# Optimization experiments

Measured on AMD Instinct MI355X. Metric: run time of the kernel, lower is better.

Reference implementation:

```python
import jax, jax.numpy as jnp
import numpy as np

B, N, D = 4, 2048, 2048
H, KVH, DH = 16, 4, 128  # query heads, kv heads (GQA), head dim
SCALE = DH ** -0.5
NEG = -jnp.finfo(jnp.float32).max


def setup_inputs() -> dict:
    key = jax.random.key(0)
    ks = jax.random.split(key, 5)
    s = 1.0 / np.sqrt(D)  # fan-in scaling for bias-free Linear weights
    return {
        "x": jax.random.normal(ks[0], (B, N, D), dtype=jnp.float32),
        "Wq": jax.random.normal(ks[1], (D, H * DH), dtype=jnp.float32) * s,
        "Wk": jax.random.normal(ks[2], (D, KVH * DH), dtype=jnp.float32) * s,
        "Wv": jax.random.normal(ks[3], (D, KVH * DH), dtype=jnp.float32) * s,
        "Wo": jax.random.normal(ks[4], (H * DH, D), dtype=jnp.float32) * s,
    }


def reference(x, Wq, Wk, Wv, Wo):
    # projections (bias-free Linear), split into heads: b n (h d) -> b h n d
    q = (x @ Wq).reshape(B, N, H, DH).transpose(0, 2, 1, 3)
    k = (x @ Wk).reshape(B, N, KVH, DH).transpose(0, 2, 1, 3)
    v = (x @ Wv).reshape(B, N, KVH, DH).transpose(0, 2, 1, 3)
    # GQA head repeat: 'b kvh n d -> b (r kvh) n d' with r outermost == tile
    r = H // KVH
    k = jnp.tile(k, (1, r, 1, 1))
    v = jnp.tile(v, (1, r, 1, 1))
    # scaled dot-product attention, causal triu(1) mask, softmax in fp32
    dots = jnp.einsum("bhid,bhjd->bhij", q, k) * SCALE
    causal_mask = jnp.triu(jnp.ones((N, N), dtype=bool), k=1)
    dots = jnp.where(causal_mask, NEG, dots)
    attn = jax.nn.softmax(dots.astype(jnp.float32), axis=-1).astype(dots.dtype)
    out = jnp.einsum("bhij,bhjd->bhid", attn, v)
    # merge heads: b h n d -> b n (h d), then output projection
    out = out.transpose(0, 2, 1, 3).reshape(B, N, H * DH)
    return out @ Wo
```

## Files before the change

kernel.cpp:

```cpp
#include <hip/hip_runtime.h>

#define B_   4
#define N_   2048
#define D_   2048
#define H_   16
#define KVH_ 4
#define DH_  128
#define SCALE_ 0.08838834764831845f
#define NEGF_ (-1.0e30f)

typedef __bf16 bf16x8 __attribute__((ext_vector_type(8)));
typedef float  f32x4  __attribute__((ext_vector_type(4)));
typedef unsigned short ushort_t;

typedef __attribute__((address_space(1))) const void* gas_cp;
typedef __attribute__((address_space(3))) void* las_p;

__device__ __forceinline__ void gload_lds16(const void* g, void* l) {
  __builtin_amdgcn_global_load_lds((gas_cp)g, (las_p)l, 16, 0, 0);
}

__device__ __forceinline__ ushort_t f2bf(float f) {
  union { float f; unsigned u; } c;
  c.f = f;
  unsigned u = c.u;
  u += 0x7fffu + ((u >> 16) & 1u);
  return (ushort_t)(u >> 16);
}

__device__ __forceinline__ float bf2f(ushort_t u) {
  union { unsigned u; float f; } c;
  c.u = ((unsigned)u) << 16;
  return c.f;
}

__global__ __launch_bounds__(256) void cvt_f32_bf16_k(
    const float* __restrict__ in, ushort_t* __restrict__ out, int n) {
  int i = (blockIdx.x * 256 + threadIdx.x) * 4;
  if (i >= n) return;
  float4 v = *reinterpret_cast<const float4*>(in + i);
  ushort4 o;
  o.x = f2bf(v.x); o.y = f2bf(v.y); o.z = f2bf(v.z); o.w = f2bf(v.w);
  *reinterpret_cast<ushort4*>(out + i) = o;
}

__global__ __launch_bounds__(256) void tconv_k(
    const float* __restrict__ src, ushort_t* __restrict__ dst, int K, int N) {
  __shared__ float tile[32][33];
  int n0 = blockIdx.x * 32, k0 = blockIdx.y * 32;
  int tx = threadIdx.x, ty = threadIdx.y;
#pragma unroll
  for (int i = 0; i < 32; i += 8)
    tile[ty + i][tx] = src[(size_t)(k0 + ty + i) * N + n0 + tx];
  __syncthreads();
#pragma unroll
  for (int i = 0; i < 32; i += 8)
    dst[(size_t)(n0 + ty + i) * K + k0 + tx] = f2bf(tile[tx][ty + i]);
}

__global__ __launch_bounds__(256) void vt_k(
    const ushort_t* __restrict__ qkv, ushort_t* __restrict__ vtg) {
  __shared__ ushort_t tile[32][33];
  int n0 = blockIdx.x * 32, d0 = blockIdx.y * 32, g = blockIdx.z;
  int b = g >> 2, kvh = g & 3;
  int tx = threadIdx.x, ty = threadIdx.y;
  const ushort_t* src = qkv + (size_t)(b * N_) * 3072 + 2560 + kvh * 128;
#pragma unroll
  for (int i = 0; i < 32; i += 8)
    tile[ty + i][tx] = src[(size_t)(n0 + ty + i) * 3072 + d0 + tx];
  __syncthreads();
  ushort_t* dst = vtg + (size_t)(g * 128) * 2048;
#pragma unroll
  for (int i = 0; i < 32; i += 8)
    dst[(size_t)(d0 + ty + i) * 2048 + n0 + tx] = tile[tx][ty + i];
}

template <int OUTF32>
__global__ __launch_bounds__(256, 2) void gemm_bt_k(
    const ushort_t* __restrict__ A, const ushort_t* __restrict__ Bt,
    void* __restrict__ C, int M, int N, int K) {
  __shared__ ushort_t As[128 * 64];
  __shared__ ushort_t Bs[128 * 64];
  const int tid = threadIdx.x;
  const int wave = tid >> 6, lane = tid & 63;
  const int lo = lane & 15, hi = lane >> 4;
  const int wm = wave >> 1, wn = wave & 1;
  const int nwg = gridDim.x * gridDim.y;
  const int id = blockIdx.y * gridDim.x + blockIdx.x;
  const int swz = (id & 7) * (nwg >> 3) + (id >> 3);
  const int m0 = (swz / gridDim.x) * 128, n0 = (swz % gridDim.x) * 128;

  f32x4 acc[4][4] = {};

  const int sr = lane >> 3;
  const int sc = lane & 7;

  const int kTiles = K >> 6;
  for (int kt = 0; kt < kTiles; ++kt) {
    const int k0 = kt << 6;
    __syncthreads();
#pragma unroll
    for (int j = 0; j < 4; ++j) {
      int r = wave * 32 + j * 8 + sr;
      int cs = sc ^ (r & 7);
      gload_lds16(A  + (size_t)(m0 + r) * K + k0 + cs * 8, As + (wave * 32 + j * 8) * 64);
      gload_lds16(Bt + (size_t)(n0 + r) * K + k0 + cs * 8, Bs + (wave * 32 + j * 8) * 64);
    }
    __syncthreads();
#pragma unroll
    for (int ks = 0; ks < 2; ++ks) {
      bf16x8 af[4], bfr[4];
#pragma unroll
      for (int mi = 0; mi < 4; ++mi) {
        int r = wm * 64 + mi * 16 + lo;
        int cs = ((ks << 2) | hi) ^ (r & 7);
        af[mi] = *reinterpret_cast<const bf16x8*>(As + r * 64 + cs * 8);
      }
#pragma unroll
      for (int ni = 0; ni < 4; ++ni) {
        int r = wn * 64 + ni * 16 + lo;
        int cs = ((ks << 2) | hi) ^ (r & 7);
        bfr[ni] = *reinterpret_cast<const bf16x8*>(Bs + r * 64 + cs * 8);
      }
#pragma unroll
      for (int mi = 0; mi < 4; ++mi)
#pragma unroll
        for (int ni = 0; ni < 4; ++ni)
          acc[mi][ni] = __builtin_amdgcn_mfma_f32_16x16x32_bf16(af[mi], bfr[ni], acc[mi][ni], 0, 0, 0);
    }
  }
#pragma unroll
  for (int mi = 0; mi < 4; ++mi) {
#pragma unroll
    for (int ni = 0; ni < 4; ++ni) {
#pragma unroll
      for (int r = 0; r < 4; ++r) {
        int row = m0 + wm * 64 + mi * 16 + hi * 4 + r;
        int col = n0 + wn * 64 + ni * 16 + lo;
        float v = acc[mi][ni][r];
        if (OUTF32) reinterpret_cast<float*>(C)[(size_t)row * N + col] = v;
        else        reinterpret_cast<ushort_t*>(C)[(size_t)row * N + col] = f2bf(v);
      }
    }
  }
}

__global__ __launch_bounds__(256, 2) void attn_k(
    const ushort_t* __restrict__ qkv, const ushort_t* __restrict__ vtg,
    ushort_t* __restrict__ ob) {
  __shared__ ushort_t Ks[2][64 * 128];
  __shared__ ushort_t Vs[2][128 * 64];
  __shared__ ushort_t Pl[4][32 * 40];

  const int nqb = gridDim.x - 1 - blockIdx.x;
  const int bh = blockIdx.y;
  const int b = bh >> 4, h = bh & 15, kvh = h & 3;
  const int tid = threadIdx.x, wave = tid >> 6, lane = tid & 63;
  const int lo = lane & 15, hi = lane >> 4;
  const int q0w = nqb * 128 + wave * 32;

  const ushort_t* qbase = qkv + (size_t)(b * N_) * 3072;
  const ushort_t* kbase = qbase + 2048 + kvh * 128;
  const ushort_t* vbase = vtg + (size_t)((b * 4 + kvh) * 128) * 2048;

  bf16x8 qf[2][4];
#pragma unroll
  for (int mi = 0; mi < 2; ++mi) {
    const ushort_t* qrow = qbase + (size_t)(q0w + mi * 16 + lo) * 3072 + h * 128;
#pragma unroll
    for (int kf = 0; kf < 4; ++kf) {
      union { bf16x8 v; ushort_t s[8]; } t;
      t.v = *reinterpret_cast<const bf16x8*>(qrow + kf * 32 + hi * 8);
#pragma unroll
      for (int j = 0; j < 8; ++j) t.s[j] = f2bf(bf2f(t.s[j]) * SCALE_);
      qf[mi][kf] = t.v;
    }
  }

  float m[2] = {NEGF_, NEGF_};
  float l[2] = {0.f, 0.f};
  f32x4 o[2][8] = {};

  const int nk = (nqb + 1) * 2;

  auto STAGE = [&](int k0, int bufi) {
#pragma unroll
    for (int j = 0; j < 4; ++j) {
      int ci = j * 256 + tid;
      int r = ci >> 4, c = ci & 15;
      gload_lds16(kbase + (size_t)(k0 + r) * 3072 + (c ^ (r & 7)) * 8,
                  &Ks[bufi][(j * 256 + wave * 64) * 8]);
    }
#pragma unroll
    for (int j = 0; j < 4; ++j) {
      int ci = j * 256 + tid;
      int r = ci >> 3, c = ci & 7;
      gload_lds16(vbase + (size_t)r * 2048 + k0 + (c ^ (r & 7)) * 8,
                  &Vs[bufi][(j * 256 + wave * 64) * 8]);
    }
  };

  STAGE(0, 0);
  __syncthreads();
  int cur = 0;

  for (int kt = 0; kt < nk; ++kt) {
    const int k0 = kt * 64;
    if (kt + 1 < nk) STAGE(k0 + 64, cur ^ 1);

    const bool act = (k0 < q0w + 32);
    if (act) {
      f32x4 s[2][4] = {};
#pragma unroll
      for (int cf = 0; cf < 4; ++cf) {
        int r = cf * 16 + lo;
        bf16x8 kb[4];
#pragma unroll
        for (int kf = 0; kf < 4; ++kf) {
          int cc = ((kf << 2) | hi) ^ (r & 7);
          kb[kf] = *reinterpret_cast<const bf16x8*>(&Ks[cur][r * 128 + cc * 8]);
        }
#pragma unroll
        for (int mi = 0; mi < 2; ++mi)
#pragma unroll
          for (int kf = 0; kf < 4; ++kf)
            s[mi][cf] = __builtin_amdgcn_mfma_f32_16x16x32_bf16(kb[kf], qf[mi][kf], s[mi][cf], 0, 0, 0);
      }
#pragma unroll
      for (int mi = 0; mi < 2; ++mi) {
        const int qrow = q0w + mi * 16 + lo;
        const bool domask = (k0 + 63 > q0w + mi * 16);
        float mx = NEGF_;
#pragma unroll
        for (int cf = 0; cf < 4; ++cf)
#pragma unroll
          for (int r = 0; r < 4; ++r) {
            float v = s[mi][cf][r];
            if (domask && (k0 + cf * 16 + hi * 4 + r > qrow)) v = NEGF_;
            s[mi][cf][r] = v;
            mx = fmaxf(mx, v);
          }
        mx = fmaxf(mx, __shfl_xor(mx, 16, 64));
        mx = fmaxf(mx, __shfl_xor(mx, 32, 64));
        float mn = fmaxf(m[mi], mx);
        float sc = __expf(m[mi] - mn);
        m[mi] = mn;
        float ps = 0.f;
#pragma unroll
        for (int cf = 0; cf < 4; ++cf)
#pragma unroll
          for (int r = 0; r < 4; ++r) {
            float p = __expf(s[mi][cf][r] - mn);
            ps += p;
            s[mi][cf][r] = p;
          }
        ps += __shfl_xor(ps, 16, 64);
        ps += __shfl_xor(ps, 32, 64);
        l[mi] = l[mi] * sc + ps;
        int bsrc = (lane & 48) | (hi << 2);
#pragma unroll
        for (int r = 0; r < 4; ++r) {
          float sb = __shfl(sc, bsrc + r, 64);
#pragma unroll
          for (int f = 0; f < 8; ++f) o[mi][f][r] *= sb;
        }
      }
#pragma unroll
      for (int ks = 0; ks < 2; ++ks) {
#pragma unroll
        for (int mi = 0; mi < 2; ++mi)
#pragma unroll
          for (int c2 = 0; c2 < 2; ++c2) {
            int cf = ks * 2 + c2;
            unsigned w0 = (unsigned)f2bf(s[mi][cf][0]) | ((unsigned)f2bf(s[mi][cf][1]) << 16);
            unsigned w1 = (unsigned)f2bf(s[mi][cf][2]) | ((unsigned)f2bf(s[mi][cf][3]) << 16);
            uint2 w; w.x = w0; w.y = w1;
            *reinterpret_cast<uint2*>(&Pl[wave][(mi * 16 + lo) * 40 + c2 * 16 + hi * 4]) = w;
          }
        bf16x8 pa[2];
#pragma unroll
        for (int mi = 0; mi < 2; ++mi)
          pa[mi] = *reinterpret_cast<const bf16x8*>(&Pl[wave][(mi * 16 + lo) * 40 + hi * 8]);
#pragma unroll
        for (int f = 0; f < 8; ++f) {
          int d = f * 16 + lo;
          int cc = ((ks << 2) | hi) ^ (d & 7);
          bf16x8 vb = *reinterpret_cast<const bf16x8*>(&Vs[cur][d * 64 + cc * 8]);
#pragma unroll
          for (int mi = 0; mi < 2; ++mi)
            o[mi][f] = __builtin_amdgcn_mfma_f32_16x16x32_bf16(pa[mi], vb, o[mi][f], 0, 0, 0);
        }
      }
    }
    __syncthreads();
    cur ^= 1;
  }

  ushort_t* obase = ob + (size_t)(b * N_ + q0w) * 2048 + h * 128;
#pragma unroll
  for (int mi = 0; mi < 2; ++mi) {
    float invl = 1.0f / l[mi];
    int bsrc = (lane & 48) | (hi << 2);
    float ib[4];
#pragma unroll
    for (int r = 0; r < 4; ++r) ib[r] = __shfl(invl, bsrc + r, 64);
#pragma unroll
    for (int f = 0; f < 8; ++f)
#pragma unroll
      for (int r = 0; r < 4; ++r)
        obase[(size_t)(mi * 16 + hi * 4 + r) * 2048 + f * 16 + lo] = f2bf(o[mi][f][r] * ib[r]);
  }
}

extern "C" void kernel_launch(void* const* d_in, const int* in_sizes, int n_in,
                              void* d_out, int out_size, void* d_ws, size_t ws_size,
                              hipStream_t stream) {
  const float* x  = (const float*)d_in[0];
  const float* Wq = (const float*)d_in[1];
  const float* Wk = (const float*)d_in[2];
  const float* Wv = (const float*)d_in[3];
  const float* Wo = (const float*)d_in[4];
  float* out = (float*)d_out;

  ushort_t* xb   = (ushort_t*)d_ws;
  ushort_t* w1t  = xb  + 16777216;
  ushort_t* wot  = w1t + 6291456;
  ushort_t* qkv  = wot + 4194304;
  ushort_t* obuf = xb;
  ushort_t* vtg  = w1t;

  cvt_f32_bf16_k<<<16384, 256, 0, stream>>>(x, xb, 16777216);
  dim3 tb(32, 8);
  tconv_k<<<dim3(64, 64), tb, 0, stream>>>(Wq, w1t,               2048, 2048);
  tconv_k<<<dim3(16, 64), tb, 0, stream>>>(Wk, w1t + 2048 * 2048, 2048, 512);
  tconv_k<<<dim3(16, 64), tb, 0, stream>>>(Wv, w1t + 2560 * 2048, 2048, 512);
  tconv_k<<<dim3(64, 64), tb, 0, stream>>>(Wo, wot,               2048, 2048);

  gemm_bt_k<0><<<dim3(24, 64), 256, 0, stream>>>(xb, w1t, qkv, 8192, 3072, 2048);
  vt_k<<<dim3(64, 4, 16), tb, 0, stream>>>(qkv, vtg);
  attn_k<<<dim3(16, 64), 256, 0, stream>>>(qkv, vtg, obuf);
  gemm_bt_k<1><<<dim3(16, 64), 256, 0, stream>>>(obuf, wot, out, 8192, 2048, 2048);
}
```

Measured before the change: 558.9 us.

## Pair causal query blocks per workgroup, add lazy rescale, setprio and packed bf16 convert

Each attention workgroup now handles two query blocks, a heavy one (15-b) and a light one (b), so causal work is balanced across workgroups and the grid is halved. The online softmax skips rescaling of the accumulator when the new row max stays within a threshold of the running max, which saves exp and multiply work. MFMA sections are wrapped in s_setprio, and P is converted to bf16 with the v_cvt_pk_bf16_f32 instruction. The halved grid (512 workgroups) may lower occupancy or parallelism, and the lazy rescale gives up some numerical headroom.

```diff
diff --git a/kernel.cpp b/kernel.cpp
--- a/kernel.cpp
+++ b/kernel.cpp
@@ -152,36 +152,14 @@
   __shared__ ushort_t Vs[2][128 * 64];
   __shared__ ushort_t Pl[4][32 * 40];
 
-  const int nqb = gridDim.x - 1 - blockIdx.x;
   const int bh = blockIdx.y;
   const int b = bh >> 4, h = bh & 15, kvh = h & 3;
   const int tid = threadIdx.x, wave = tid >> 6, lane = tid & 63;
   const int lo = lane & 15, hi = lane >> 4;
-  const int q0w = nqb * 128 + wave * 32;
 
   const ushort_t* qbase = qkv + (size_t)(b * N_) * 3072;
   const ushort_t* kbase = qbase + 2048 + kvh * 128;
   const ushort_t* vbase = vtg + (size_t)((b * 4 + kvh) * 128) * 2048;
-
-  bf16x8 qf[2][4];
-#pragma unroll
-  for (int mi = 0; mi < 2; ++mi) {
-    const ushort_t* qrow = qbase + (size_t)(q0w + mi * 16 + lo) * 3072 + h * 128;
-#pragma unroll
-    for (int kf = 0; kf < 4; ++kf) {
-      union { bf16x8 v; ushort_t s[8]; } t;
-      t.v = *reinterpret_cast<const bf16x8*>(qrow + kf * 32 + hi * 8);
-#pragma unroll
-      for (int j = 0; j < 8; ++j) t.s[j] = f2bf(bf2f(t.s[j]) * SCALE_);
-      qf[mi][kf] = t.v;
-    }
-  }
-
-  float m[2] = {NEGF_, NEGF_};
-  float l[2] = {0.f, 0.f};
-  f32x4 o[2][8] = {};
-
-  const int nk = (nqb + 1) * 2;
 
   auto STAGE = [&](int k0, int bufi) {
 #pragma unroll
@@ -200,115 +178,158 @@
     }
   };
 
-  STAGE(0, 0);
-  __syncthreads();
-  int cur = 0;
-
-  for (int kt = 0; kt < nk; ++kt) {
-    const int k0 = kt * 64;
-    if (kt + 1 < nk) STAGE(k0 + 64, cur ^ 1);
-
-    const bool act = (k0 < q0w + 32);
-    if (act) {
-      f32x4 s[2][4] = {};
-#pragma unroll
-      for (int cf = 0; cf < 4; ++cf) {
-        int r = cf * 16 + lo;
-        bf16x8 kb[4];
-#pragma unroll
-        for (int kf = 0; kf < 4; ++kf) {
-          int cc = ((kf << 2) | hi) ^ (r & 7);
-          kb[kf] = *reinterpret_cast<const bf16x8*>(&Ks[cur][r * 128 + cc * 8]);
+#pragma unroll 1
+  for (int pass = 0; pass < 2; ++pass) {
+    const int nqb = pass ? blockIdx.x : (15 - blockIdx.x);
+    const int q0w = nqb * 128 + wave * 32;
+
+    bf16x8 qf[2][4];
+#pragma unroll
+    for (int mi = 0; mi < 2; ++mi) {
+      const ushort_t* qrow = qbase + (size_t)(q0w + mi * 16 + lo) * 3072 + h * 128;
+#pragma unroll
+      for (int kf = 0; kf < 4; ++kf) {
+        union { bf16x8 v; ushort_t s[8]; } t;
+        t.v = *reinterpret_cast<const bf16x8*>(qrow + kf * 32 + hi * 8);
+#pragma unroll
+        for (int j = 0; j < 8; ++j) t.s[j] = f2bf(bf2f(t.s[j]) * SCALE_);
+        qf[mi][kf] = t.v;
+      }
+    }
+
+    float m[2] = {NEGF_, NEGF_};
+    float l[2] = {0.f, 0.f};
+    f32x4 o[2][8] = {};
+
+    const int nk = (nqb + 1) * 2;
+
+    STAGE(0, 0);
+    __syncthreads();
+    int cur = 0;
+
+    for (int kt = 0; kt < nk; ++kt) {
+      const int k0 = kt * 64;
+      if (kt + 1 < nk) STAGE(k0 + 64, cur ^ 1);
+
+      const bool act = (k0 < q0w + 32);
+      if (act) {
+        f32x4 s[2][4] = {};
+        __builtin_amdgcn_s_setprio(1);
+#pragma unroll
+        for (int cf = 0; cf < 4; ++cf) {
+          int r = cf * 16 + lo;
+          bf16x8 kb[4];
+#pragma unroll
+          for (int kf = 0; kf < 4; ++kf) {
+            int cc = ((kf << 2) | hi) ^ (r & 7);
+            kb[kf] = *reinterpret_cast<const bf16x8*>(&Ks[cur][r * 128 + cc * 8]);
+          }
+#pragma unroll
+          for (int mi = 0; mi < 2; ++mi)
+#pragma unroll
+            for (int kf = 0; kf < 4; ++kf)
+              s[mi][cf] = __builtin_amdgcn_mfma_f32_16x16x32_bf16(kb[kf], qf[mi][kf], s[mi][cf], 0, 0, 0);
         }
-#pragma unroll
-        for (int mi = 0; mi < 2; ++mi)
-#pragma unroll
-          for (int kf = 0; kf < 4; ++kf)
-            s[mi][cf] = __builtin_amdgcn_mfma_f32_16x16x32_bf16(kb[kf], qf[mi][kf], s[mi][cf], 0, 0, 0);
-      }
-#pragma unroll
-      for (int mi = 0; mi < 2; ++mi) {
-        const int qrow = q0w + mi * 16 + lo;
-        const bool domask = (k0 + 63 > q0w + mi * 16);
-        float mx = NEGF_;
-#pragma unroll
-        for (int cf = 0; cf < 4; ++cf)
-#pragma unroll
-          for (int r = 0; r < 4; ++r) {
-            float v = s[mi][cf][r];
-            if (domask && (k0 + cf * 16 + hi * 4 + r > qrow)) v = NEGF_;
-            s[mi][cf][r] = v;
-            mx = fmaxf(mx, v);
+        __builtin_amdgcn_s_setprio(0);
+#pragma unroll
+        for (int mi = 0; mi < 2; ++mi) {
+          const int qrow = q0w + mi * 16 + lo;
+          const bool domask = (k0 + 63 > q0w + mi * 16);
+          float mx = NEGF_;
+#pragma unroll
+          for (int cf = 0; cf < 4; ++cf)
+#pragma unroll
+            for (int r = 0; r < 4; ++r) {
+              float v = s[mi][cf][r];
+              if (domask && (k0 + cf * 16 + hi * 4 + r > qrow)) v = NEGF_;
+              s[mi][cf][r] = v;
+              mx = fmaxf(mx, v);
+            }
+          mx = fmaxf(mx, __shfl_xor(mx, 16, 64));
+          mx = fmaxf(mx, __shfl_xor(mx, 32, 64));
+          const bool noresc = __all(mx <= m[mi] + 8.0f);
+          float mn, sc;
+          if (noresc) {
+            mn = m[mi];
+          } else {
+            mn = fmaxf(m[mi], mx);
+            sc = __expf(m[mi] - mn);
+            m[mi] = mn;
           }
-        mx = fmaxf(mx, __shfl_xor(mx, 16, 64));
-        mx = fmaxf(mx, __shfl_xor(mx, 32, 64));
-        float mn = fmaxf(m[mi], mx);
-        float sc = __expf(m[mi] - mn);
-        m[mi] = mn;
-        float ps = 0.f;
-#pragma unroll
-        for (int cf = 0; cf < 4; ++cf)
-#pragma unroll
-          for (int r = 0; r < 4; ++r) {
-            float p = __expf(s[mi][cf][r] - mn);
-            ps += p;
-            s[mi][cf][r] = p;
+          float ps = 0.f;
+#pragma unroll
+          for (int cf = 0; cf < 4; ++cf)
+#pragma unroll
+            for (int r = 0; r < 4; ++r) {
+              float p = __expf(s[mi][cf][r] - mn);
+              ps += p;
+              s[mi][cf][r] = p;
+            }
+          ps += __shfl_xor(ps, 16, 64);
+          ps += __shfl_xor(ps, 32, 64);
+          if (noresc) {
+            l[mi] += ps;
+          } else {
+            l[mi] = l[mi] * sc + ps;
+            int bsrc = (lane & 48) | (hi << 2);
+#pragma unroll
+            for (int r = 0; r < 4; ++r) {
+              float sb = __shfl(sc, bsrc + r, 64);
+#pragma unroll
+              for (int f = 0; f < 8; ++f) o[mi][f][r] *= sb;
+            }
           }
-        ps += __shfl_xor(ps, 16, 64);
-        ps += __shfl_xor(ps, 32, 64);
-        l[mi] = l[mi] * sc + ps;
-        int bsrc = (lane & 48) | (hi << 2);
-#pragma unroll
-        for (int r = 0; r < 4; ++r) {
-          float sb = __shfl(sc, bsrc + r, 64);
-#pragma unroll
-          for (int f = 0; f < 8; ++f) o[mi][f][r] *= sb;
         }
-      }
-#pragma unroll
-      for (int ks = 0; ks < 2; ++ks) {
-#pragma unroll
-        for (int mi = 0; mi < 2; ++mi)
-#pragma unroll
-          for (int c2 = 0; c2 < 2; ++c2) {
-            int cf = ks * 2 + c2;
-            unsigned w0 = (unsigned)f2bf(s[mi][cf][0]) | ((unsigned)f2bf(s[mi][cf][1]) << 16);
-            unsigned w1 = (unsigned)f2bf(s[mi][cf][2]) | ((unsigned)f2bf(s[mi][cf][3]) << 16);
-            uint2 w; w.x = w0; w.y = w1;
-            *reinterpret_cast<uint2*>(&Pl[wave][(mi * 16 + lo) * 40 + c2 * 16 + hi * 4]) = w;
+#pragma unroll
+        for (int ks = 0; ks < 2; ++ks) {
+#pragma unroll
+          for (int mi = 0; mi < 2; ++mi)
+#pragma unroll
+            for (int c2 = 0; c2 < 2; ++c2) {
+              int cf = ks * 2 + c2;
+              unsigned w0, w1;
+              asm("v_cvt_pk_bf16_f32 %0, %1, %2"
+                  : "=v"(w0) : "v"(s[mi][cf][0]), "v"(s[mi][cf][1]));
+              asm("v_cvt_pk_bf16_f32 %0, %1, %2"
+                  : "=v"(w1) : "v"(s[mi][cf][2]), "v"(s[mi][cf][3]));
+              uint2 w; w.x = w0; w.y = w1;
+              *reinterpret_cast<uint2*>(&Pl[wave][(mi * 16 + lo) * 40 + c2 * 16 + hi * 4]) = w;
+            }
+          bf16x8 pa[2];
+#pragma unroll
+          for (int mi = 0; mi < 2; ++mi)
+            pa[mi] = *reinterpret_cast<const bf16x8*>(&Pl[wave][(mi * 16 + lo) * 40 + hi * 8]);
+          __builtin_amdgcn_s_setprio(1);
+#pragma unroll
+          for (int f = 0; f < 8; ++f) {
+            int d = f * 16 + lo;
+            int cc = ((ks << 2) | hi) ^ (d & 7);
+            bf16x8 vb = *reinterpret_cast<const bf16x8*>(&Vs[cur][d * 64 + cc * 8]);
+#pragma unroll
+            for (int mi = 0; mi < 2; ++mi)
+              o[mi][f] = __builtin_amdgcn_mfma_f32_16x16x32_bf16(pa[mi], vb, o[mi][f], 0, 0, 0);
           }
-        bf16x8 pa[2];
-#pragma unroll
-        for (int mi = 0; mi < 2; ++mi)
-          pa[mi] = *reinterpret_cast<const bf16x8*>(&Pl[wave][(mi * 16 + lo) * 40 + hi * 8]);
-#pragma unroll
-        for (int f = 0; f < 8; ++f) {
-          int d = f * 16 + lo;
-          int cc = ((ks << 2) | hi) ^ (d & 7);
-          bf16x8 vb = *reinterpret_cast<const bf16x8*>(&Vs[cur][d * 64 + cc * 8]);
-#pragma unroll
-          for (int mi = 0; mi < 2; ++mi)
-            o[mi][f] = __builtin_amdgcn_mfma_f32_16x16x32_bf16(pa[mi], vb, o[mi][f], 0, 0, 0);
+          __builtin_amdgcn_s_setprio(0);
         }
       }
-    }
-    __syncthreads();
-    cur ^= 1;
-  }
-
-  ushort_t* obase = ob + (size_t)(b * N_ + q0w) * 2048 + h * 128;
-#pragma unroll
-  for (int mi = 0; mi < 2; ++mi) {
-    float invl = 1.0f / l[mi];
-    int bsrc = (lane & 48) | (hi << 2);
-    float ib[4];
-#pragma unroll
-    for (int r = 0; r < 4; ++r) ib[r] = __shfl(invl, bsrc + r, 64);
-#pragma unroll
-    for (int f = 0; f < 8; ++f)
-#pragma unroll
-      for (int r = 0; r < 4; ++r)
-        obase[(size_t)(mi * 16 + hi * 4 + r) * 2048 + f * 16 + lo] = f2bf(o[mi][f][r] * ib[r]);
+      __syncthreads();
+      cur ^= 1;
+    }
+
+    ushort_t* obase = ob + (size_t)(b * N_ + q0w) * 2048 + h * 128;
+#pragma unroll
+    for (int mi = 0; mi < 2; ++mi) {
+      float invl = 1.0f / l[mi];
+      int bsrc = (lane & 48) | (hi << 2);
+      float ib[4];
+#pragma unroll
+      for (int r = 0; r < 4; ++r) ib[r] = __shfl(invl, bsrc + r, 64);
+#pragma unroll
+      for (int f = 0; f < 8; ++f)
+#pragma unroll
+        for (int r = 0; r < 4; ++r)
+          obase[(size_t)(mi * 16 + hi * 4 + r) * 2048 + f * 16 + lo] = f2bf(o[mi][f][r] * ib[r]);
+    }
   }
 }
 
@@ -338,6 +359,6 @@
 
   gemm_bt_k<0><<<dim3(24, 64), 256, 0, stream>>>(xb, w1t, qkv, 8192, 3072, 2048);
   vt_k<<<dim3(64, 4, 16), tb, 0, stream>>>(qkv, vtg);
-  attn_k<<<dim3(16, 64), 256, 0, stream>>>(qkv, vtg, obuf);
+  attn_k<<<dim3(8, 64), 256, 0, stream>>>(qkv, vtg, obuf);
   gemm_bt_k<1><<<dim3(16, 64), 256, 0, stream>>>(obuf, wot, out, 8192, 2048, 2048);
 }
```

Result: faster. 447.5 us (-19.9%).
